# Kernel tuning notes

Hardware: AMD Instinct MI355X
Metric: run time of the kernel (lower is better)

The kernel has to match this reference:

```python
import jax, jax.numpy as jnp
import numpy as np

NODE = 7  # feature count must equal Dense width for final broadcast


def setup_inputs() -> dict:
    key = jax.random.key(0)
    ks = jax.random.split(key, 5)
    B, N = 2048, 4096
    q = jax.random.normal(ks[0], (B, N), dtype=jnp.float32)
    k = jax.random.normal(ks[1], (B, N), dtype=jnp.float32)  # unused by the layer (overwritten), kept for fidelity
    v = jax.random.normal(ks[2], (B, N), dtype=jnp.float32)
    # Dense(node) on last-dim-1 input: kernel [1, node], bias [node]
    wq_w = jax.random.normal(ks[3], (1, NODE), dtype=jnp.float32) * 0.5
    wq_b = jnp.zeros((NODE,), jnp.float32)
    # Dense(node) on 7 features: kernel [7, node], bias [node]
    wk_w = jax.random.normal(ks[4], (NODE, NODE), dtype=jnp.float32) * (1.0 / np.sqrt(NODE))
    wk_b = jnp.zeros((NODE,), jnp.float32)
    return dict(q=q, k=k, v=v, wq_w=wq_w, wq_b=wq_b, wk_w=wk_w, wk_b=wk_b)


def _signed_root(x, r):
    # tf: pow(abs(x), 1/r) * sign(x)
    return jnp.sign(x) * jnp.abs(x) ** (1.0 / r)


def reference(q, k, v, wq_w, wq_b, wk_w, wk_b):
    B, N = v.shape
    # power sums over the set axis (VP), computed once (kept as [B,1], tiling deferred)
    p1 = jnp.sum(v, axis=-1, keepdims=True)
    p2 = jnp.sum(v * v, axis=-1, keepdims=True)
    p3 = jnp.sum(v ** 3, axis=-1, keepdims=True)
    p4 = jnp.sum(v ** 4, axis=-1, keepdims=True)
    # Newton's identities -> elementary symmetric polynomials (VC1..VC4)
    e1 = p1
    e2 = (p1 ** 2 - p2) / 2
    e3 = (p1 ** 3 - p3 - 3 * (p2 * p1 - p3)) / 6
    e4 = (e3 * p1 - e2 * p2 + e1 * p3 - p4) / 4
    # signed roots as in original; vc1 is left un-rooted
    f = jnp.concatenate(
        [e1,
         _signed_root(e2, 2), _signed_root(e3, 3), _signed_root(e4, 4),
         _signed_root(p2, 2), _signed_root(p3, 3), _signed_root(p4, 4)],
        axis=-1)  # [B, 7]
    # tf.tile broadcasts each feature across the set axis -> [B, N, 7]
    vfeat = jnp.broadcast_to(f[:, None, :], (B, N, f.shape[-1]))

    # q path: expand_dims(-1) then Dense(node): [B,N,1] @ [1,7] + b -> [B,N,7]
    qe = q[..., None] * wq_w[0] + wq_b
    # k path: Dense(node) on features: [B,N,7] @ [7,7] + b
    ke = vfeat @ wk_w + wk_b

    # original transposes to [B,7,N] and L2-normalizes over the last (set) axis;
    # equivalently normalize over axis=1 without transposing
    def norm_over_set(x):
        nrm = jnp.sqrt(jnp.sum(x * x, axis=1, keepdims=True)) + 1e-10
        return x / nrm

    qn = norm_over_set(qe)
    kn = norm_over_set(ke)

    w = kn * qn              # multiply_no_nan(k, q); finite inputs -> plain multiply
    out = jnp.sum(w * vfeat, axis=-1)  # [B, N]
    return out
```

## Files before the change

### kernel.cpp

```cpp
#include <hip/hip_runtime.h>
#include <math.h>


constexpr int NTH = 256;
constexpr int NN  = 4096;

__device__ inline double sroot2(double x) {
    return copysign(sqrt(fabs(x)), x);
}
__device__ inline double sroot4(double x) {
    return copysign(sqrt(sqrt(fabs(x))), x);
}
__device__ inline double sroot3(double x) {
    double a = fabs(x);
    if (a < 1e-300) return 0.0;
    double y = (double)exp2f(log2f((float)a) * (1.0f / 3.0f));
    y = (2.0 * y + a / (y * y)) * (1.0 / 3.0);
    y = (2.0 * y + a / (y * y)) * (1.0 / 3.0);
    return copysign(y, x);
}

__global__ __launch_bounds__(NTH) void symm_set_basis_kernel(
    const float* __restrict__ q,
    const float* __restrict__ v,
    const float* __restrict__ wq_w,
    const float* __restrict__ wq_b,
    const float* __restrict__ wk_w,
    const float* __restrict__ wk_b,
    float* __restrict__ out)
{
    const int b = blockIdx.x;
    const int t = threadIdx.x;
    const float4* q4 = (const float4*)(q + (size_t)b * NN);
    const float4* v4 = (const float4*)(v + (size_t)b * NN);
    float4*       o4 = (float4*)(out + (size_t)b * NN);

    float4 qv[4], vv[4];
    #pragma unroll
    for (int i = 0; i < 4; ++i) {
        qv[i] = q4[t + i * NTH];
        vv[i] = v4[t + i * NTH];
    }

    float p1 = 0.f, p2 = 0.f, p3 = 0.f, p4 = 0.f, s1 = 0.f, s2 = 0.f;
    #pragma unroll
    for (int i = 0; i < 4; ++i) {
        const float xs[4] = {vv[i].x, vv[i].y, vv[i].z, vv[i].w};
        const float qs[4] = {qv[i].x, qv[i].y, qv[i].z, qv[i].w};
        #pragma unroll
        for (int j = 0; j < 4; ++j) {
            const float x  = xs[j];
            const float x2 = x * x;
            p1 += x;
            p2 += x2;
            p3 += x2 * x;
            p4 += x2 * x2;
            const float qq = qs[j];
            s1 += qq;
            s2 += qq * qq;
        }
    }

    double r[6] = {(double)p1, (double)p2, (double)p3, (double)p4,
                   (double)s1, (double)s2};
    #pragma unroll
    for (int off = 32; off > 0; off >>= 1) {
        #pragma unroll
        for (int k = 0; k < 6; ++k) r[k] += __shfl_down(r[k], off, 64);
    }

    __shared__ double red[4][6];
    __shared__ float  AD[2];
    const int wave = t >> 6, lane = t & 63;
    if (lane == 0) {
        #pragma unroll
        for (int k = 0; k < 6; ++k) red[wave][k] = r[k];
    }
    __syncthreads();

    if (wave == 0) {
        double tot[6];
        #pragma unroll
        for (int k = 0; k < 6; ++k)
            tot[k] = red[0][k] + red[1][k] + red[2][k] + red[3][k];

        const double P1 = tot[0], P2 = tot[1], P3 = tot[2], P4 = tot[3];
        const double S1 = tot[4], S2 = tot[5];

        const double e1 = P1;
        const double e2 = (P1 * P1 - P2) * 0.5;
        const double e3 = (P1 * P1 * P1 - P3 - 3.0 * (P2 * P1 - P3)) / 6.0;
        const double e4 = (e3 * P1 - e2 * P2 + e1 * P3 - P4) * 0.25;

        double f[7];
        f[0] = e1;
        f[1] = sroot2(e2);
        f[2] = sroot3(e3);
        f[3] = sroot4(e4);
        f[4] = sroot2(P2);
        f[5] = sroot3(P3);
        f[6] = sroot4(P4);

        double ke[7];
        #pragma unroll
        for (int j = 0; j < 7; ++j) {
            double acc = (double)wk_b[j];
            #pragma unroll
            for (int i = 0; i < 7; ++i) acc += f[i] * (double)wk_w[i * 7 + j];
            ke[j] = acc;
        }

        const double sqrtN = sqrt((double)NN);
        double A = 0.0, D = 0.0;
        #pragma unroll
        for (int j = 0; j < 7; ++j) {
            const double wj  = (double)wq_w[j];
            const double bj  = (double)wq_b[j];
            const double knj = ke[j] / (sqrtN * fabs(ke[j]) + 1e-10);
            const double nq  = sqrt(wj * wj * S2 + 2.0 * wj * bj * S1 +
                                    (double)NN * bj * bj) + 1e-10;
            const double g = knj * f[j] / nq;
            A += g * wj;
            D += g * bj;
        }
        if (lane == 0) {
            AD[0] = (float)A;
            AD[1] = (float)D;
        }
    }
    __syncthreads();

    const float Af = AD[0], Df = AD[1];

    #pragma unroll
    for (int i = 0; i < 4; ++i) {
        float4 o;
        o.x = qv[i].x * Af + Df;
        o.y = qv[i].y * Af + Df;
        o.z = qv[i].z * Af + Df;
        o.w = qv[i].w * Af + Df;
        o4[t + i * NTH] = o;
    }
}

extern "C" void kernel_launch(void* const* d_in, const int* in_sizes, int n_in,
                              void* d_out, int out_size, void* d_ws, size_t ws_size,
                              hipStream_t stream) {
    const float* q    = (const float*)d_in[0];
    const float* v    = (const float*)d_in[2];
    const float* wq_w = (const float*)d_in[3];
    const float* wq_b = (const float*)d_in[4];
    const float* wk_w = (const float*)d_in[5];
    const float* wk_b = (const float*)d_in[6];
    float* out = (float*)d_out;

    const int B = in_sizes[0] / NN;
    symm_set_basis_kernel<<<B, NTH, 0, stream>>>(q, v, wq_w, wq_b, wk_w, wk_b, out);
}
```

Before: 135.9 us.

## Split fused kernel into reduce, per-row epilogue, and apply kernels

Splits the single fused kernel into three launches. The first reduces power sums per wave in float and writes partials to workspace. The second computes the double-precision scalar epilogue with one thread per row. The third re-reads q and applies the affine map. The intent is to take the serial double-precision epilogue and its block syncs off the bandwidth-bound path, at the cost of reading q a second time, two extra launches, and dropping the double-precision shuffle reduction.

```diff
diff --git a/kernel.cpp b/kernel.cpp
--- a/kernel.cpp
+++ b/kernel.cpp
@@ -5,41 +5,22 @@
 constexpr int NTH = 256;
 constexpr int NN  = 4096;
 
-__device__ inline double sroot2(double x) {
-    return copysign(sqrt(fabs(x)), x);
-}
-__device__ inline double sroot4(double x) {
-    return copysign(sqrt(sqrt(fabs(x))), x);
-}
-__device__ inline double sroot3(double x) {
-    double a = fabs(x);
-    if (a < 1e-300) return 0.0;
-    double y = (double)exp2f(log2f((float)a) * (1.0f / 3.0f));
-    y = (2.0 * y + a / (y * y)) * (1.0 / 3.0);
-    y = (2.0 * y + a / (y * y)) * (1.0 / 3.0);
-    return copysign(y, x);
-}
-
-__global__ __launch_bounds__(NTH) void symm_set_basis_kernel(
+__global__ __launch_bounds__(NTH) void k1_reduce(
     const float* __restrict__ q,
     const float* __restrict__ v,
-    const float* __restrict__ wq_w,
-    const float* __restrict__ wq_b,
-    const float* __restrict__ wk_w,
-    const float* __restrict__ wk_b,
-    float* __restrict__ out)
+    float* __restrict__ part)
 {
     const int b = blockIdx.x;
     const int t = threadIdx.x;
-    const float4* q4 = (const float4*)(q + (size_t)b * NN);
-    const float4* v4 = (const float4*)(v + (size_t)b * NN);
-    float4*       o4 = (float4*)(out + (size_t)b * NN);
+    const int w = t >> 6, l = t & 63;
+    const float4* q4 = (const float4*)(q + (size_t)b * NN) + (w << 8);
+    const float4* v4 = (const float4*)(v + (size_t)b * NN) + (w << 8);
 
     float4 qv[4], vv[4];
     #pragma unroll
     for (int i = 0; i < 4; ++i) {
-        qv[i] = q4[t + i * NTH];
-        vv[i] = v4[t + i * NTH];
+        qv[i] = q4[l + (i << 6)];
+        vv[i] = v4[l + (i << 6)];
     }
 
     float p1 = 0.f, p2 = 0.f, p3 = 0.f, p4 = 0.f, s1 = 0.f, s2 = 0.f;
@@ -51,95 +32,115 @@
         for (int j = 0; j < 4; ++j) {
             const float x  = xs[j];
             const float x2 = x * x;
-            p1 += x;
-            p2 += x2;
-            p3 += x2 * x;
-            p4 += x2 * x2;
+            p1 += x;  p2 += x2;  p3 += x2 * x;  p4 += x2 * x2;
             const float qq = qs[j];
-            s1 += qq;
-            s2 += qq * qq;
+            s1 += qq; s2 += qq * qq;
         }
     }
 
-    double r[6] = {(double)p1, (double)p2, (double)p3, (double)p4,
-                   (double)s1, (double)s2};
+    float r[6] = {p1, p2, p3, p4, s1, s2};
     #pragma unroll
     for (int off = 32; off > 0; off >>= 1) {
         #pragma unroll
         for (int k = 0; k < 6; ++k) r[k] += __shfl_down(r[k], off, 64);
     }
+    if (l == 0) {
+        float* o = part + ((size_t)b * 4 + w) * 6;
+        #pragma unroll
+        for (int k = 0; k < 6; ++k) o[k] = r[k];
+    }
+}
 
-    __shared__ double red[4][6];
-    __shared__ float  AD[2];
-    const int wave = t >> 6, lane = t & 63;
-    if (lane == 0) {
+__device__ inline double sroot2(double x) { return copysign(sqrt(fabs(x)), x); }
+__device__ inline double sroot4(double x) { return copysign(sqrt(sqrt(fabs(x))), x); }
+__device__ inline double sroot3(double x) {
+    double a = fabs(x);
+    if (a < 1e-300) return 0.0;
+    double y = (double)exp2f(log2f((float)a) * (1.0f / 3.0f));
+    y = (2.0 * y + a / (y * y)) * (1.0 / 3.0);
+    y = (2.0 * y + a / (y * y)) * (1.0 / 3.0);
+    return copysign(y, x);
+}
+
+__global__ __launch_bounds__(NTH) void k2_epilogue(
+    const float* __restrict__ part,
+    const float* __restrict__ wq_w,
+    const float* __restrict__ wq_b,
+    const float* __restrict__ wk_w,
+    const float* __restrict__ wk_b,
+    float2* __restrict__ AD,
+    int B)
+{
+    const int b = blockIdx.x * NTH + threadIdx.x;
+    if (b >= B) return;
+    const float* pp = part + (size_t)b * 24;
+
+    double tot[6];
+    #pragma unroll
+    for (int k = 0; k < 6; ++k)
+        tot[k] = (double)pp[k] + (double)pp[6 + k] +
+                 (double)pp[12 + k] + (double)pp[18 + k];
+
+    const double P1 = tot[0], P2 = tot[1], P3 = tot[2], P4 = tot[3];
+    const double S1 = tot[4], S2 = tot[5];
+
+    const double e1 = P1;
+    const double e2 = (P1 * P1 - P2) * 0.5;
+    const double e3 = (P1 * P1 * P1 - P3 - 3.0 * (P2 * P1 - P3)) / 6.0;
+    const double e4 = (e3 * P1 - e2 * P2 + e1 * P3 - P4) * 0.25;
+
+    double f[7];
+    f[0] = e1;
+    f[1] = sroot2(e2);
+    f[2] = sroot3(e3);
+    f[3] = sroot4(e4);
+    f[4] = sroot2(P2);
+    f[5] = sroot3(P3);
+    f[6] = sroot4(P4);
+
+    double ke[7];
+    #pragma unroll
+    for (int j = 0; j < 7; ++j) {
+        double acc = (double)wk_b[j];
         #pragma unroll
-        for (int k = 0; k < 6; ++k) red[wave][k] = r[k];
+        for (int i = 0; i < 7; ++i) acc += f[i] * (double)wk_w[i * 7 + j];
+        ke[j] = acc;
     }
-    __syncthreads();
 
-    if (wave == 0) {
-        double tot[6];
-        #pragma unroll
-        for (int k = 0; k < 6; ++k)
-            tot[k] = red[0][k] + red[1][k] + red[2][k] + red[3][k];
+    const double sqrtN = sqrt((double)NN);
+    double A = 0.0, D = 0.0;
+    #pragma unroll
+    for (int j = 0; j < 7; ++j) {
+        const double wj  = (double)wq_w[j];
+        const double bj  = (double)wq_b[j];
+        const double knj = ke[j] / (sqrtN * fabs(ke[j]) + 1e-10);
+        const double nq  = sqrt(wj * wj * S2 + 2.0 * wj * bj * S1 +
+                                (double)NN * bj * bj) + 1e-10;
+        const double g = knj * f[j] / nq;
+        A += g * wj;
+        D += g * bj;
+    }
+    AD[b] = make_float2((float)A, (float)D);
+}
 
-        const double P1 = tot[0], P2 = tot[1], P3 = tot[2], P4 = tot[3];
-        const double S1 = tot[4], S2 = tot[5];
-
-        const double e1 = P1;
-        const double e2 = (P1 * P1 - P2) * 0.5;
-        const double e3 = (P1 * P1 * P1 - P3 - 3.0 * (P2 * P1 - P3)) / 6.0;
-        const double e4 = (e3 * P1 - e2 * P2 + e1 * P3 - P4) * 0.25;
-
-        double f[7];
-        f[0] = e1;
-        f[1] = sroot2(e2);
-        f[2] = sroot3(e3);
-        f[3] = sroot4(e4);
-        f[4] = sroot2(P2);
-        f[5] = sroot3(P3);
-        f[6] = sroot4(P4);
-
-        double ke[7];
-        #pragma unroll
-        for (int j = 0; j < 7; ++j) {
-            double acc = (double)wk_b[j];
-            #pragma unroll
-            for (int i = 0; i < 7; ++i) acc += f[i] * (double)wk_w[i * 7 + j];
-            ke[j] = acc;
-        }
-
-        const double sqrtN = sqrt((double)NN);
-        double A = 0.0, D = 0.0;
-        #pragma unroll
-        for (int j = 0; j < 7; ++j) {
-            const double wj  = (double)wq_w[j];
-            const double bj  = (double)wq_b[j];
-            const double knj = ke[j] / (sqrtN * fabs(ke[j]) + 1e-10);
-            const double nq  = sqrt(wj * wj * S2 + 2.0 * wj * bj * S1 +
-                                    (double)NN * bj * bj) + 1e-10;
-            const double g = knj * f[j] / nq;
-            A += g * wj;
-            D += g * bj;
-        }
-        if (lane == 0) {
-            AD[0] = (float)A;
-            AD[1] = (float)D;
-        }
-    }
-    __syncthreads();
-
-    const float Af = AD[0], Df = AD[1];
-
+__global__ __launch_bounds__(NTH) void k3_apply(
+    const float* __restrict__ q,
+    const float2* __restrict__ AD,
+    float* __restrict__ out)
+{
+    const int b = blockIdx.x;
+    const int t = threadIdx.x;
+    const float2 ad = AD[b];
+    const float A = ad.x, D = ad.y;
+    const float4* q4 = (const float4*)(q + (size_t)b * NN);
+    float4*       o4 = (float4*)(out + (size_t)b * NN);
     #pragma unroll
     for (int i = 0; i < 4; ++i) {
+        float4 x = q4[t + (i << 8)];
         float4 o;
-        o.x = qv[i].x * Af + Df;
-        o.y = qv[i].y * Af + Df;
-        o.z = qv[i].z * Af + Df;
-        o.w = qv[i].w * Af + Df;
-        o4[t + i * NTH] = o;
+        o.x = x.x * A + D;  o.y = x.y * A + D;
+        o.z = x.z * A + D;  o.w = x.w * A + D;
+        o4[t + (i << 8)] = o;
     }
 }
 
@@ -155,5 +156,12 @@
     float* out = (float*)d_out;
 
     const int B = in_sizes[0] / NN;
-    symm_set_basis_kernel<<<B, NTH, 0, stream>>>(q, v, wq_w, wq_b, wk_w, wk_b, out);
+
+    float*  part = (float*)d_ws;
+    float2* AD   = (float2*)((char*)d_ws + (size_t)B * 24 * sizeof(float));
+
+    k1_reduce  <<<B, NTH, 0, stream>>>(q, v, part);
+    k2_epilogue<<<(B + NTH - 1) / NTH, NTH, 0, stream>>>(part, wq_w, wq_b,
+                                                         wk_w, wk_b, AD, B);
+    k3_apply   <<<B, NTH, 0, stream>>>(q, AD, out);
 }
```

Result: slower. 140.1 us (+3.1%).
